# Kernel tuning notes

Measured on AMD Instinct MI355X. Metric: run time of the kernel, lower is better.

Reference implementation:

```python
import jax, jax.numpy as jnp
import numpy as np

T, D, H, L = 4096, 1024, 512, 2  # seq_len, input_size, per-direction hidden (state_size//2), num_layers


def setup_inputs() -> dict:
    key = jax.random.key(0)
    inp = {"emb": jax.random.normal(key, (T, D), jnp.float32) * 0.1}
    k = 1
    for d in ("fwd", "bwd"):
        for l in range(L):
            in_sz = D if l == 0 else H
            inp[f"{d}_Wih_{l}"] = jax.random.normal(jax.random.fold_in(key, k), (4 * H, in_sz), jnp.float32) * float(1.0 / np.sqrt(in_sz)); k += 1
            inp[f"{d}_Whh_{l}"] = jax.random.normal(jax.random.fold_in(key, k), (4 * H, H), jnp.float32) * float(1.0 / np.sqrt(H)); k += 1
            inp[f"{d}_bih_{l}"] = jnp.zeros((4 * H,), jnp.float32)
            inp[f"{d}_bhh_{l}"] = jnp.zeros((4 * H,), jnp.float32)
    return inp


def _lstm_stack(xs, params):
    """Run a stack of unidirectional LSTM layers over xs [T, in].
    Returns (final cells [L,H], final hiddens [L,H], top-layer outputs [T,H])."""
    cTs, hTs = [], []
    for Wih, Whh, bih, bhh in params:
        h0 = jnp.zeros((Wih.shape[0] // 4,), xs.dtype)

        def step(carry, x, Wih=Wih, Whh=Whh, b=bih + bhh):
            h, c = carry
            g = Wih @ x + Whh @ h + b          # [4H], torch LSTMCell gate order i,f,g,o
            i, f, gg, o = jnp.split(g, 4)
            c = jax.nn.sigmoid(f) * c + jax.nn.sigmoid(i) * jnp.tanh(gg)
            h = jax.nn.sigmoid(o) * jnp.tanh(c)
            return (h, c), h

        (hT, cT), xs = jax.lax.scan(step, (h0, h0), xs)
        cTs.append(cT)
        hTs.append(hT)
    return jnp.stack(cTs), jnp.stack(hTs), xs


def reference(emb,
              fwd_Wih_0, fwd_Whh_0, fwd_bih_0, fwd_bhh_0,
              fwd_Wih_1, fwd_Whh_1, fwd_bih_1, fwd_bhh_1,
              bwd_Wih_0, bwd_Whh_0, bwd_bih_0, bwd_bhh_0,
              bwd_Wih_1, bwd_Whh_1, bwd_bih_1, bwd_bhh_1):
    fparams = [(fwd_Wih_0, fwd_Whh_0, fwd_bih_0, fwd_bhh_0),
               (fwd_Wih_1, fwd_Whh_1, fwd_bih_1, fwd_bhh_1)]
    bparams = [(bwd_Wih_0, bwd_Whh_0, bwd_bih_0, bwd_bhh_0),
               (bwd_Wih_1, bwd_Whh_1, bwd_bih_1, bwd_bhh_1)]
    fc, fh, fy = _lstm_stack(emb, fparams)          # forward pass over sequence
    bc, bh, by = _lstm_stack(emb[::-1], bparams)    # backward pass over reversed sequence
    cell_memories = jnp.concatenate([fc, bc], axis=-1)   # [L, state_size]
    hidden_states = jnp.concatenate([fh, bh], axis=-1)   # [L, state_size]
    outputs = jnp.concatenate([fy, by[::-1]], axis=-1)   # [T, state_size] per-token final-layer states
    return (cell_memories, hidden_states, outputs)
```

## Files before the change

### kernel.cpp

```cpp
#include <hip/hip_runtime.h>
#include <cstdint>
#include <cstddef>

#define T_SEQ 4096
#define HSZ   512
#define NGATE 2048
#define DIN   1024
#define NB0   16
#define HB0   32
#define NB1   32
#define HB1   16
#define S_SLOT 16
#define CH    132

typedef unsigned long long u64;
typedef unsigned int u32;

__device__ __forceinline__ u64 exld(const u64* p) {
  return __hip_atomic_load(p, __ATOMIC_RELAXED, __HIP_MEMORY_SCOPE_AGENT);
}
__device__ __forceinline__ void exst(u64* p, u64 v) {
  __hip_atomic_store(p, v, __ATOMIC_RELAXED, __HIP_MEMORY_SCOPE_AGENT);
}
__device__ __forceinline__ int pgld(const u32* p) {
  return (int)__hip_atomic_load(p, __ATOMIC_RELAXED, __HIP_MEMORY_SCOPE_AGENT);
}
__device__ __forceinline__ void pgst(u32* p, u32 v) {
  __hip_atomic_store(p, v, __ATOMIC_RELAXED, __HIP_MEMORY_SCOPE_AGENT);
}

__device__ __forceinline__ float frcp(float x) { return __builtin_amdgcn_rcpf(x); }
__device__ __forceinline__ float fsig(float x) { return frcp(1.f + __expf(-x)); }
__device__ __forceinline__ float ftnh(float x) { return 1.f - 2.f * frcp(1.f + __expf(2.f * x)); }

__global__ void init_sync_kernel(u64* ex, u32* prog) {
  const int tid = blockIdx.x * blockDim.x + threadIdx.x;
  if (tid < 2 * 2 * S_SLOT * HSZ) exst(&ex[tid], 0ull);
  if (tid < 2 * (NB0 + NB1)) pgst(&prog[tid], 0u);
}

__global__ __launch_bounds__(256, 2)
void gemm_bias_kernel(const float* __restrict__ Xf, const float* __restrict__ Xb,
                      const float* __restrict__ Wf, const float* __restrict__ Wb,
                      const float* __restrict__ bif, const float* __restrict__ bhf,
                      const float* __restrict__ bib, const float* __restrict__ bhb,
                      float* __restrict__ Pf, float* __restrict__ Pb, int K)
{
  const int dir = blockIdx.z;
  const float* X  = dir ? Xb  : Xf;
  const float* W  = dir ? Wb  : Wf;
  const float* bi = dir ? bib : bif;
  const float* bh = dir ? bhb : bhf;
  float* P        = dir ? Pb  : Pf;

  const int m0 = blockIdx.x * 128;
  const int n0 = blockIdx.y * 128;
  const int tid = threadIdx.x;
  const int lr = tid >> 1;
  const int lk = (tid & 1) * 8;

  __shared__ float As[16*128];
  __shared__ float Bs[16*128];

  float acc[8][8];
  #pragma unroll
  for (int i = 0; i < 8; ++i)
    #pragma unroll
    for (int j = 0; j < 8; ++j) acc[i][j] = 0.f;

  for (int k0 = 0; k0 < K; k0 += 16) {
    const float4 a0 = *(const float4*)(X + (size_t)(m0+lr)*K + k0 + lk);
    const float4 a1 = *(const float4*)(X + (size_t)(m0+lr)*K + k0 + lk + 4);
    const float4 b0 = *(const float4*)(W + (size_t)(n0+lr)*K + k0 + lk);
    const float4 b1 = *(const float4*)(W + (size_t)(n0+lr)*K + k0 + lk + 4);
    __syncthreads();
    As[(lk+0)*128+lr]=a0.x; As[(lk+1)*128+lr]=a0.y; As[(lk+2)*128+lr]=a0.z; As[(lk+3)*128+lr]=a0.w;
    As[(lk+4)*128+lr]=a1.x; As[(lk+5)*128+lr]=a1.y; As[(lk+6)*128+lr]=a1.z; As[(lk+7)*128+lr]=a1.w;
    Bs[(lk+0)*128+lr]=b0.x; Bs[(lk+1)*128+lr]=b0.y; Bs[(lk+2)*128+lr]=b0.z; Bs[(lk+3)*128+lr]=b0.w;
    Bs[(lk+4)*128+lr]=b1.x; Bs[(lk+5)*128+lr]=b1.y; Bs[(lk+6)*128+lr]=b1.z; Bs[(lk+7)*128+lr]=b1.w;
    __syncthreads();
    #pragma unroll
    for (int kk = 0; kk < 16; ++kk) {
      const float4 A0 = *(const float4*)(As + kk*128 + (tid&15)*8);
      const float4 A1 = *(const float4*)(As + kk*128 + (tid&15)*8 + 4);
      const float4 B0 = *(const float4*)(Bs + kk*128 + (tid>>4)*8);
      const float4 B1 = *(const float4*)(Bs + kk*128 + (tid>>4)*8 + 4);
      const float av[8] = {A0.x,A0.y,A0.z,A0.w,A1.x,A1.y,A1.z,A1.w};
      const float bv[8] = {B0.x,B0.y,B0.z,B0.w,B1.x,B1.y,B1.z,B1.w};
      #pragma unroll
      for (int i = 0; i < 8; ++i)
        #pragma unroll
        for (int j = 0; j < 8; ++j) acc[i][j] += av[i]*bv[j];
    }
  }
  const int tm = m0 + (tid&15)*8;
  const int tn = n0 + (tid>>4)*8;
  #pragma unroll
  for (int i = 0; i < 8; ++i) {
    #pragma unroll
    for (int j = 0; j < 8; ++j) {
      const int n = tn + j;
      P[(size_t)(tm+i)*NGATE + n] = acc[i][j] + bi[n] + bh[n];
    }
  }
}

__global__ __launch_bounds__(512, 2)
void fused_recur_kernel(const float* __restrict__ Whh0_f, const float* __restrict__ Whh0_b,
                        const float* __restrict__ Wih1_f, const float* __restrict__ Whh1_f,
                        const float* __restrict__ bih1_f, const float* __restrict__ bhh1_f,
                        const float* __restrict__ Wih1_b, const float* __restrict__ Whh1_b,
                        const float* __restrict__ bih1_b, const float* __restrict__ bhh1_b,
                        const float* __restrict__ P_f, const float* __restrict__ P_b,
                        u64* ex0, u64* ex1, u32* prog0, u32* prog1,
                        float* __restrict__ out)
{
  const int bx  = blockIdx.x;
  const int tid = threadIdx.x;
  const int lane = tid & 63;
  const int wv   = tid >> 6;

  __shared__ float xh[8*CH];
  __shared__ float gates[128];

  if (bx < 2*NB0) {
    const int dir = (bx >= NB0) ? 1 : 0;
    const int b   = bx - dir*NB0;
    const float* Whh = dir ? Whh0_b : Whh0_f;
    const float* P   = dir ? P_b    : P_f;
    u64* exS   = ex0 + (size_t)dir*S_SLOT*HSZ;
    u32* prS   = prog0 + dir*NB0;
    u32* prL1  = prog1 + dir*NB1;

    const int cc        = lane >> 4;
    const int row_local = wv*16 + (lane & 15);
    const int gate = row_local >> 5, k = row_local & 31;
    const int grow = gate*HSZ + b*HB0 + k;
    const bool wr  = (lane >> 4) == 0;

    float4 w[32];
    {
      const float4* wp = (const float4*)(Whh + (size_t)grow*HSZ + cc*128);
      #pragma unroll
      for (int j = 0; j < 32; ++j) w[j] = wp[j];
    }

    float creg = 0.f;
    float pv = 0.f;
    if (wr) pv = P[(size_t)(dir ? (T_SEQ-1) : 0)*NGATE + grow];

    for (int t = 0; t < T_SEQ; ++t) {
      if ((t & 7) == 0) {
        if (tid >= 64 && tid < 64+NB0)       { while (pgld(&prS[tid-64])  < t-4) {} }
        else if (tid >= 96 && tid < 96+NB1)  { while (pgld(&prL1[tid-96]) < t-4) {} }
      }
      {
        const u64* sp = exS + (size_t)(t & (S_SLOT-1))*HSZ + tid;
        u64 v;
        do { v = exld(sp); } while ((u32)(v >> 32) != (u32)t);
        xh[(tid>>7)*CH + (tid & 127)] = __uint_as_float((u32)v);
      }
      __syncthreads();
      if (tid == 0) pgst(&prS[b], (u32)(t+1));
      float pvn = 0.f;
      if (wr && t+1 < T_SEQ) pvn = P[(size_t)(dir ? (T_SEQ-2-t) : (t+1))*NGATE + grow];
      const float4* h4 = (const float4*)(xh + cc*CH);
      float a0=0.f, a1=0.f, a2=0.f, a3=0.f;
      #pragma unroll
      for (int j = 0; j < 32; j += 4) {
        const float4 h0 = h4[j], h1 = h4[j+1], h2 = h4[j+2], h3 = h4[j+3];
        a0 += w[j].x*h0.x   + w[j].y*h0.y   + w[j].z*h0.z   + w[j].w*h0.w;
        a1 += w[j+1].x*h1.x + w[j+1].y*h1.y + w[j+1].z*h1.z + w[j+1].w*h1.w;
        a2 += w[j+2].x*h2.x + w[j+2].y*h2.y + w[j+2].z*h2.z + w[j+2].w*h2.w;
        a3 += w[j+3].x*h3.x + w[j+3].y*h3.y + w[j+3].z*h3.z + w[j+3].w*h3.w;
      }
      float acc = (a0+a1)+(a2+a3);
      acc += __shfl_xor(acc, 16);
      acc += __shfl_xor(acc, 32);
      if (wr) gates[row_local] = acc + pv;
      pv = pvn;
      __syncthreads();
      if (tid < HB0) {
        const float ig = gates[tid], fg = gates[32+tid], gg = gates[64+tid], og = gates[96+tid];
        const float i_s = fsig(ig);
        const float f_s = fsig(fg);
        const float o_s = fsig(og);
        creg = f_s*creg + i_s*ftnh(gg);
        const float hnew = o_s*ftnh(creg);
        const int hidx = b*HB0 + tid;
        const u64 pkt = ((u64)(u32)(t+1) << 32) | (u64)__float_as_uint(hnew);
        exst(exS + (size_t)((t+1) & (S_SLOT-1))*HSZ + hidx, pkt);
        if (t == T_SEQ-1) {
          out[dir*HSZ + hidx]        = creg;
          out[2048 + dir*HSZ + hidx] = hnew;
        }
      }
    }
  } else {
    const int r   = bx - 2*NB0;
    const int dir = (r >= NB1) ? 1 : 0;
    const int b   = r - dir*NB1;
    const float* Wih = dir ? Wih1_b : Wih1_f;
    const float* Whh = dir ? Whh1_b : Whh1_f;
    const float* bi  = dir ? bih1_b : bih1_f;
    const float* bh  = dir ? bhh1_b : bhh1_f;
    u64* exX = ex0 + (size_t)dir*S_SLOT*HSZ;
    u64* exS = ex1 + (size_t)dir*S_SLOT*HSZ;
    u32* prS = prog1 + dir*NB1;

    const int sub       = lane >> 3;
    const int row_local = wv*8 + (lane & 7);
    const int gate = row_local >> 4, k = row_local & 15;
    const int grow = gate*HSZ + b*HB1 + k;
    const bool wr  = (lane >> 3) == 0;

    float4 w[32];
    {
      const float* wsrc = (sub < 4) ? (Wih + (size_t)grow*HSZ + sub*128)
                                    : (Whh + (size_t)grow*HSZ + (sub-4)*128);
      const float4* wp = (const float4*)wsrc;
      #pragma unroll
      for (int j = 0; j < 32; ++j) w[j] = wp[j];
    }
    float brow = 0.f;
    if (wr) brow = bi[grow] + bh[grow];

    float creg = 0.f;
    u64 xpf = exld(exX + (size_t)(1 & (S_SLOT-1))*HSZ + tid);

    for (int t = 0; t < T_SEQ; ++t) {
      if ((t & 7) == 0 && tid >= 64 && tid < 64+NB1) { while (pgld(&prS[tid-64]) < t-4) {} }
      {
        const u64* px = exX + (size_t)((t+1) & (S_SLOT-1))*HSZ + tid;
        const u64* ph = exS + (size_t)(t & (S_SLOT-1))*HSZ + tid;
        u64 vx = xpf; bool okx = ((u32)(vx >> 32) == (u32)(t+1));
        float hv = 0.f; bool okh = false;
        do {
          if (!okx) { u64 v = exld(px); if ((u32)(v >> 32) == (u32)(t+1)) { vx = v; okx = true; } }
          if (!okh) { u64 v = exld(ph); if ((u32)(v >> 32) == (u32)t)     { hv = __uint_as_float((u32)v); okh = true; } }
        } while (!(okx && okh));
        xh[(tid>>7)*CH + (tid & 127)]       = __uint_as_float((u32)vx);
        xh[(4 + (tid>>7))*CH + (tid & 127)] = hv;
      }
      __syncthreads();
      if (tid == 0) pgst(&prS[b], (u32)(t+1));
      xpf = exld(exX + (size_t)((t+2) & (S_SLOT-1))*HSZ + tid);
      const float4* v4 = (const float4*)(xh + sub*CH);
      float a0=0.f, a1=0.f, a2=0.f, a3=0.f;
      #pragma unroll
      for (int j = 0; j < 32; j += 4) {
        const float4 h0 = v4[j], h1 = v4[j+1], h2 = v4[j+2], h3 = v4[j+3];
        a0 += w[j].x*h0.x   + w[j].y*h0.y   + w[j].z*h0.z   + w[j].w*h0.w;
        a1 += w[j+1].x*h1.x + w[j+1].y*h1.y + w[j+1].z*h1.z + w[j+1].w*h1.w;
        a2 += w[j+2].x*h2.x + w[j+2].y*h2.y + w[j+2].z*h2.z + w[j+2].w*h2.w;
        a3 += w[j+3].x*h3.x + w[j+3].y*h3.y + w[j+3].z*h3.z + w[j+3].w*h3.w;
      }
      float acc = (a0+a1)+(a2+a3);
      acc += __shfl_xor(acc, 8);
      acc += __shfl_xor(acc, 16);
      acc += __shfl_xor(acc, 32);
      if (wr) gates[row_local] = acc + brow;
      __syncthreads();
      if (tid < HB1) {
        const float ig = gates[tid], fg = gates[16+tid], gg = gates[32+tid], og = gates[48+tid];
        const float i_s = fsig(ig);
        const float f_s = fsig(fg);
        const float o_s = fsig(og);
        creg = f_s*creg + i_s*ftnh(gg);
        const float hnew = o_s*ftnh(creg);
        const int hidx = b*HB1 + tid;
        const u64 pkt = ((u64)(u32)(t+1) << 32) | (u64)__float_as_uint(hnew);
        exst(exS + (size_t)((t+1) & (S_SLOT-1))*HSZ + hidx, pkt);
        const int trow = dir ? (T_SEQ-1-t) : t;
        out[4096 + (size_t)trow*1024 + dir*HSZ + hidx] = hnew;
        if (t == T_SEQ-1) {
          out[1024 + dir*HSZ + hidx]        = creg;
          out[2048 + 1024 + dir*HSZ + hidx] = hnew;
        }
      }
    }
  }
}

extern "C" void kernel_launch(void* const* d_in, const int* in_sizes, int n_in,
                              void* d_out, int out_size, void* d_ws, size_t ws_size,
                              hipStream_t stream)
{
  const float* emb   = (const float*)d_in[0];
  const float* fWih0 = (const float*)d_in[1];
  const float* fWhh0 = (const float*)d_in[2];
  const float* fbih0 = (const float*)d_in[3];
  const float* fbhh0 = (const float*)d_in[4];
  const float* fWih1 = (const float*)d_in[5];
  const float* fWhh1 = (const float*)d_in[6];
  const float* fbih1 = (const float*)d_in[7];
  const float* fbhh1 = (const float*)d_in[8];
  const float* bWih0 = (const float*)d_in[9];
  const float* bWhh0 = (const float*)d_in[10];
  const float* bbih0 = (const float*)d_in[11];
  const float* bbhh0 = (const float*)d_in[12];
  const float* bWih1 = (const float*)d_in[13];
  const float* bWhh1 = (const float*)d_in[14];
  const float* bbih1 = (const float*)d_in[15];
  const float* bbhh1 = (const float*)d_in[16];
  float* out = (float*)d_out;

  float* P_f = (float*)d_ws;
  float* P_b = P_f + (size_t)T_SEQ*NGATE;
  u64*   ex0 = (u64*)(P_b + (size_t)T_SEQ*NGATE);
  u64*   ex1 = ex0 + 2*S_SLOT*HSZ;
  u32*   prog0 = (u32*)(ex1 + 2*S_SLOT*HSZ);
  u32*   prog1 = prog0 + 2*NB0;

  init_sync_kernel<<<32, 1024, 0, stream>>>(ex0, prog0);

  gemm_bias_kernel<<<dim3(32,16,2), 256, 0, stream>>>(
      emb, emb, fWih0, bWih0, fbih0, fbhh0, bbih0, bbhh0, P_f, P_b, DIN);

  fused_recur_kernel<<<96, 512, 0, stream>>>(
      fWhh0, bWhh0,
      fWih1, fWhh1, fbih1, fbhh1,
      bWih1, bWhh1, bbih1, bbhh1,
      P_f, P_b, ex0, ex1, prog0, prog1, out);
}
```

Measured before the change: 7.916 ms.

## Remap gate rows so each wave finalizes its own LSTM cells, drop barrier

Rows are reassigned so the four gates of a hidden element sit in adjacent lanes of the same wave. Gate activations are computed in parallel across lanes and combined with xor shuffles, which removes the shared gates array and the second __syncthreads per timestep. The shared input buffer is double-buffered by timestep parity so the next step's writes cannot race with reads from the current step, now that the second barrier is gone. More lanes evaluate transcendentals, and the weight row mapping changes, which may affect load coalescing.

```diff
diff --git a/kernel.cpp b/kernel.cpp
--- a/kernel.cpp
+++ b/kernel.cpp
@@ -120,8 +120,7 @@
   const int lane = tid & 63;
   const int wv   = tid >> 6;
 
-  __shared__ float xh[8*CH];
-  __shared__ float gates[128];
+  __shared__ float xh[2][8*CH];
 
   if (bx < 2*NB0) {
     const int dir = (bx >= NB0) ? 1 : 0;
@@ -132,11 +131,13 @@
     u32* prS   = prog0 + dir*NB0;
     u32* prL1  = prog1 + dir*NB1;
 
-    const int cc        = lane >> 4;
-    const int row_local = wv*16 + (lane & 15);
-    const int gate = row_local >> 5, k = row_local & 31;
-    const int grow = gate*HSZ + b*HB0 + k;
-    const bool wr  = (lane >> 4) == 0;
+    const int g  = lane & 3;
+    const int el = (lane >> 2) & 3;
+    const int cc = lane >> 4;
+    const int e  = wv*4 + el;
+    const int grow = g*HSZ + b*HB0 + e;
+    const bool red0 = (cc == 0);
+    const bool pub  = red0 && (g == 0);
 
     float4 w[32];
     {
@@ -147,7 +148,7 @@
 
     float creg = 0.f;
     float pv = 0.f;
-    if (wr) pv = P[(size_t)(dir ? (T_SEQ-1) : 0)*NGATE + grow];
+    if (red0) pv = P[(size_t)(dir ? (T_SEQ-1) : 0)*NGATE + grow];
 
     for (int t = 0; t < T_SEQ; ++t) {
       if ((t & 7) == 0) {
@@ -158,13 +159,13 @@
         const u64* sp = exS + (size_t)(t & (S_SLOT-1))*HSZ + tid;
         u64 v;
         do { v = exld(sp); } while ((u32)(v >> 32) != (u32)t);
-        xh[(tid>>7)*CH + (tid & 127)] = __uint_as_float((u32)v);
+        xh[t & 1][(tid>>7)*CH + (tid & 127)] = __uint_as_float((u32)v);
       }
       __syncthreads();
       if (tid == 0) pgst(&prS[b], (u32)(t+1));
       float pvn = 0.f;
-      if (wr && t+1 < T_SEQ) pvn = P[(size_t)(dir ? (T_SEQ-2-t) : (t+1))*NGATE + grow];
-      const float4* h4 = (const float4*)(xh + cc*CH);
+      if (red0 && t+1 < T_SEQ) pvn = P[(size_t)(dir ? (T_SEQ-2-t) : (t+1))*NGATE + grow];
+      const float4* h4 = (const float4*)(xh[t & 1] + cc*CH);
       float a0=0.f, a1=0.f, a2=0.f, a3=0.f;
       #pragma unroll
       for (int j = 0; j < 32; j += 4) {
@@ -177,17 +178,16 @@
       float acc = (a0+a1)+(a2+a3);
       acc += __shfl_xor(acc, 16);
       acc += __shfl_xor(acc, 32);
-      if (wr) gates[row_local] = acc + pv;
+      const float val = acc + pv;
       pv = pvn;
-      __syncthreads();
-      if (tid < HB0) {
-        const float ig = gates[tid], fg = gates[32+tid], gg = gates[64+tid], og = gates[96+tid];
-        const float i_s = fsig(ig);
-        const float f_s = fsig(fg);
-        const float o_s = fsig(og);
-        creg = f_s*creg + i_s*ftnh(gg);
-        const float hnew = o_s*ftnh(creg);
-        const int hidx = b*HB0 + tid;
+      const float av = (g == 2) ? ftnh(val) : fsig(val);
+      const float f1 = __shfl_xor(av, 1);
+      const float f2 = __shfl_xor(av, 2);
+      const float f3 = __shfl_xor(av, 3);
+      if (pub) {
+        creg = f1*creg + av*f2;
+        const float hnew = f3*ftnh(creg);
+        const int hidx = b*HB0 + e;
         const u64 pkt = ((u64)(u32)(t+1) << 32) | (u64)__float_as_uint(hnew);
         exst(exS + (size_t)((t+1) & (S_SLOT-1))*HSZ + hidx, pkt);
         if (t == T_SEQ-1) {
@@ -208,11 +208,13 @@
     u64* exS = ex1 + (size_t)dir*S_SLOT*HSZ;
     u32* prS = prog1 + dir*NB1;
 
-    const int sub       = lane >> 3;
-    const int row_local = wv*8 + (lane & 7);
-    const int gate = row_local >> 4, k = row_local & 15;
-    const int grow = gate*HSZ + b*HB1 + k;
-    const bool wr  = (lane >> 3) == 0;
+    const int g   = lane & 3;
+    const int el  = (lane >> 2) & 1;
+    const int sub = lane >> 3;
+    const int e   = wv*2 + el;
+    const int grow = g*HSZ + b*HB1 + e;
+    const bool red0 = (sub == 0);
+    const bool pub  = red0 && (g == 0);
 
     float4 w[32];
     {
@@ -223,7 +225,7 @@
       for (int j = 0; j < 32; ++j) w[j] = wp[j];
     }
     float brow = 0.f;
-    if (wr) brow = bi[grow] + bh[grow];
+    if (red0) brow = bi[grow] + bh[grow];
 
     float creg = 0.f;
     u64 xpf = exld(exX + (size_t)(1 & (S_SLOT-1))*HSZ + tid);
@@ -239,13 +241,13 @@
           if (!okx) { u64 v = exld(px); if ((u32)(v >> 32) == (u32)(t+1)) { vx = v; okx = true; } }
           if (!okh) { u64 v = exld(ph); if ((u32)(v >> 32) == (u32)t)     { hv = __uint_as_float((u32)v); okh = true; } }
         } while (!(okx && okh));
-        xh[(tid>>7)*CH + (tid & 127)]       = __uint_as_float((u32)vx);
-        xh[(4 + (tid>>7))*CH + (tid & 127)] = hv;
+        xh[t & 1][(tid>>7)*CH + (tid & 127)]       = __uint_as_float((u32)vx);
+        xh[t & 1][(4 + (tid>>7))*CH + (tid & 127)] = hv;
       }
       __syncthreads();
       if (tid == 0) pgst(&prS[b], (u32)(t+1));
       xpf = exld(exX + (size_t)((t+2) & (S_SLOT-1))*HSZ + tid);
-      const float4* v4 = (const float4*)(xh + sub*CH);
+      const float4* v4 = (const float4*)(xh[t & 1] + sub*CH);
       float a0=0.f, a1=0.f, a2=0.f, a3=0.f;
       #pragma unroll
       for (int j = 0; j < 32; j += 4) {
@@ -259,16 +261,15 @@
       acc += __shfl_xor(acc, 8);
       acc += __shfl_xor(acc, 16);
       acc += __shfl_xor(acc, 32);
-      if (wr) gates[row_local] = acc + brow;
-      __syncthreads();
-      if (tid < HB1) {
-        const float ig = gates[tid], fg = gates[16+tid], gg = gates[32+tid], og = gates[48+tid];
-        const float i_s = fsig(ig);
-        const float f_s = fsig(fg);
-        const float o_s = fsig(og);
-        creg = f_s*creg + i_s*ftnh(gg);
-        const float hnew = o_s*ftnh(creg);
-        const int hidx = b*HB1 + tid;
+      const float val = acc + brow;
+      const float av = (g == 2) ? ftnh(val) : fsig(val);
+      const float f1 = __shfl_xor(av, 1);
+      const float f2 = __shfl_xor(av, 2);
+      const float f3 = __shfl_xor(av, 3);
+      if (pub) {
+        creg = f1*creg + av*f2;
+        const float hnew = f3*ftnh(creg);
+        const int hidx = b*HB1 + e;
         const u64 pkt = ((u64)(u32)(t+1) << 32) | (u64)__float_as_uint(hnew);
         exst(exS + (size_t)((t+1) & (S_SLOT-1))*HSZ + hidx, pkt);
         const int trow = dir ? (T_SEQ-1-t) : t;
```

Result: no change. 7.998 ms (+1.0%).
